# Kernel optimization log

Hardware: AMD Instinct MI355X
Metric: run time of the kernel (lower is better)

The kernel has to match this reference:

```python
import jax, jax.numpy as jnp
import numpy as np

EMBED = 1024  # embed_dim = hidden_dim = out_dim (n_head=1)
NQ, NK = 4096, 4096
NEG = 1e16


def setup_inputs() -> dict:
    key = jax.random.key(0)
    ks = jax.random.split(key, 10)
    stdv = 1.0 / np.sqrt(EMBED)
    lin = lambda kk: jax.random.uniform(kk, (EMBED, EMBED), jnp.float32, -stdv, stdv)
    vec = lambda kk: jax.random.uniform(kk, (EMBED,), jnp.float32, -stdv, stdv)
    return {
        "q": jax.random.normal(ks[0], (NQ, EMBED), jnp.float32),
        "k": jax.random.normal(ks[1], (NK, EMBED), jnp.float32),
        "mask": jax.random.randint(ks[2], (NQ, NK), 0, 2, jnp.int32),
        "wei": jax.random.uniform(ks[3], (NQ, NK), jnp.float32),
        "Wq": lin(ks[4]), "bq": vec(ks[5]),
        "Wk": lin(ks[6]), "bk": vec(ks[7]),
        "Wp": lin(ks[8]), "bp": vec(ks[9]),
    }


def reference(q, k, mask, wei, Wq, bq, Wk, bk, Wp, bp):
    # Linear projections (torch Linear: x @ W.T + b)
    kx = k @ Wk.T + bk                      # [NK, D]
    qx = q @ Wq.T + bq                      # [NQ, D]
    # dot_product score
    score = qx @ kx.T                       # [NQ, NK]
    bias = (mask.astype(jnp.int32) - 1).astype(score.dtype) * NEG
    score = jax.nn.softmax(score + bias, axis=-1)
    # second weighted+masked softmax pass
    score = jax.nn.softmax(score * wei + bias, axis=-1)
    out = (score @ kx) @ Wp.T + bp          # [NQ, D]
    return out, score
```

## Files before the change

### kernel.cpp

```cpp
#include <hip/hip_runtime.h>


typedef __bf16 bf16;
typedef __bf16 bf16x8 __attribute__((ext_vector_type(8)));
typedef __bf16 bf16x4 __attribute__((ext_vector_type(4)));
typedef float  f32x4  __attribute__((ext_vector_type(4)));
typedef float  f32x16 __attribute__((ext_vector_type(16)));

typedef __attribute__((address_space(1))) void as1_void;
typedef __attribute__((address_space(3))) void as3_void;

#define NQ  4096
#define NKK 4096
#define EMB 1024

#define BM 128
#define BN 128
#define BK 32

__device__ __forceinline__ void gld_lds16(const void* g, void* l) {
    __builtin_amdgcn_global_load_lds((as1_void*)g, (as3_void*)l, 16, 0, 0);
}

__global__ __launch_bounds__(256) void prep_all(
    const float* __restrict__ q, const float* __restrict__ k,
    const float* __restrict__ Wq, const float* __restrict__ Wk, const float* __restrict__ Wp,
    bf16* __restrict__ qh, bf16* __restrict__ ql,
    bf16* __restrict__ kh, bf16* __restrict__ kl,
    bf16* __restrict__ Wqh, bf16* __restrict__ Wql,
    bf16* __restrict__ Wkh, bf16* __restrict__ Wkl,
    bf16* __restrict__ Wph, bf16* __restrict__ Wpl,
    int nqk, int nw)
{
    const int z = blockIdx.y;
    const float* s; bf16* h; bf16* l; int n;
    switch (z) {
        case 0:  s = q;  h = qh;  l = ql;  n = nqk; break;
        case 1:  s = k;  h = kh;  l = kl;  n = nqk; break;
        case 2:  s = Wq; h = Wqh; l = Wql; n = nw;  break;
        case 3:  s = Wk; h = Wkh; l = Wkl; n = nw;  break;
        default: s = Wp; h = Wph; l = Wpl; n = nw;  break;
    }
    const int i = (blockIdx.x * 256 + threadIdx.x) * 4;
    if (i >= n) return;
    f32x4 v = *(const f32x4*)(s + i);
    bf16x4 hv, lv;
#pragma unroll
    for (int c = 0; c < 4; c++) {
        float x = v[c];
        bf16 hh = (bf16)x;
        hv[c] = hh;
        lv[c] = (bf16)(x - (float)hh);
    }
    *(bf16x4*)(h + i) = hv;
    *(bf16x4*)(l + i) = lv;
}

__global__ __launch_bounds__(256) void transpose_bf16(
    const bf16* __restrict__ src, bf16* __restrict__ dst, int R, int C)
{
    __shared__ bf16 tile[32][33];
    const int bx = blockIdx.x * 32;
    const int by = blockIdx.y * 32;
    const int tx = threadIdx.x & 31;
    const int ty = threadIdx.x >> 5;
#pragma unroll
    for (int r = 0; r < 4; r++)
        tile[ty + 8 * r][tx] = src[(size_t)(by + ty + 8 * r) * C + bx + tx];
    __syncthreads();
#pragma unroll
    for (int r = 0; r < 4; r++)
        dst[(size_t)(bx + ty + 8 * r) * R + by + tx] = tile[tx][ty + 8 * r];
}

template<int NS, int MODE>
__global__ __launch_bounds__(256) void reduce_k(
    const float* __restrict__ P, const float* __restrict__ bias,
    float* __restrict__ of, bf16* __restrict__ oh, int n, int Nld)
{
    const int i = (blockIdx.x * 256 + threadIdx.x) * 4;
    if (i >= n) return;
    f32x4 v = *(const f32x4*)(P + i);
#pragma unroll
    for (int s = 1; s < NS; s++)
        v += *(const f32x4*)(P + (size_t)s * n + i);
    if (MODE == 1)
        v += *(const f32x4*)(bias + (i & (Nld - 1)));
    if (MODE == 0) {
        bf16x4 o;
#pragma unroll
        for (int c = 0; c < 4; c++) o[c] = (bf16)v[c];
        *(bf16x4*)(oh + i) = o;
    } else {
        *(f32x4*)(of + i) = v;
    }
}

template<int NSPLIT, int HAS_BIAS, int OUT_BF16>
__global__ __launch_bounds__(256) void gemm_bt(
    const bf16* __restrict__ A, const bf16* __restrict__ B,
    const float* __restrict__ bias,
    float* __restrict__ Cf, bf16* __restrict__ Cb,
    int M, int N, int Ksub, int lda, int ldb)
{
    __shared__ bf16 sA[BM * BK];
    __shared__ bf16 sB[BN * BK];
    const int t    = threadIdx.x;
    const int wave = t >> 6;
    const int lane = t & 63;
    const int l31  = lane & 31;
    const int lhi  = lane >> 5;
    const int wm   = wave >> 1;
    const int wn   = wave & 1;
    const int bm   = blockIdx.y * BM;
    const int bn   = blockIdx.x * BN;
    const int srow = t >> 2;
    const int gseg = (t & 3) ^ ((srow >> 1) & 3);
    const int rsw  = (l31 >> 1) & 3;
    const int kz   = (NSPLIT > 0) ? (int)blockIdx.z : 0;

    A += (size_t)kz * Ksub;
    B += (size_t)kz * Ksub;
    if (NSPLIT > 0) Cf += (size_t)kz * M * N;

    const bf16* ga = A + (size_t)(bm + srow) * lda + gseg * 8;
    const bf16* gb = B + (size_t)(bn + srow) * ldb + gseg * 8;
    char* lA = (char*)sA + wave * 1024;
    char* lB = (char*)sB + wave * 1024;

    f32x16 acc[2][2] = {};

    for (int k0 = 0; k0 < Ksub; k0 += BK) {
        __syncthreads();
        gld_lds16(ga + k0,                      lA);
        gld_lds16(ga + (size_t)64 * lda + k0,   lA + 4096);
        gld_lds16(gb + k0,                      lB);
        gld_lds16(gb + (size_t)64 * ldb + k0,   lB + 4096);
        __syncthreads();
        bf16x8 af[2][2], bfr[2][2];
#pragma unroll
        for (int mi = 0; mi < 2; mi++)
#pragma unroll
            for (int kh = 0; kh < 2; kh++)
                af[mi][kh] = *(const bf16x8*)
                    &sA[(wm * 64 + mi * 32 + l31) * BK + ((kh * 2 + lhi) ^ rsw) * 8];
#pragma unroll
        for (int nj = 0; nj < 2; nj++)
#pragma unroll
            for (int kh = 0; kh < 2; kh++)
                bfr[nj][kh] = *(const bf16x8*)
                    &sB[(wn * 64 + nj * 32 + l31) * BK + ((kh * 2 + lhi) ^ rsw) * 8];
#pragma unroll
        for (int kh = 0; kh < 2; kh++)
#pragma unroll
            for (int mi = 0; mi < 2; mi++)
#pragma unroll
                for (int nj = 0; nj < 2; nj++)
                    acc[mi][nj] = __builtin_amdgcn_mfma_f32_32x32x16_bf16(
                        af[mi][kh], bfr[nj][kh], acc[mi][nj], 0, 0, 0);
    }

#pragma unroll
    for (int mi = 0; mi < 2; mi++)
#pragma unroll
        for (int nj = 0; nj < 2; nj++) {
            const int cg = bn + wn * 64 + nj * 32 + l31;
            const float bv = HAS_BIAS ? bias[cg] : 0.0f;
#pragma unroll
            for (int r = 0; r < 16; r++) {
                const int rg = bm + wm * 64 + mi * 32 + (r & 3) + 8 * (r >> 2) + 4 * lhi;
                const float v = acc[mi][nj][r] + bv;
                const size_t idx = (size_t)rg * N + cg;
                if (NSPLIT > 0)    Cf[idx] = v;
                else if (OUT_BF16) Cb[idx] = (bf16)v;
                else               Cf[idx] = v;
            }
        }
}

template<int BATCH, int HAS_BIAS, int HILO>
__global__ __launch_bounds__(256) void gemm_bt_split(
    const bf16* __restrict__ Ah0, const bf16* __restrict__ Al0,
    const bf16* __restrict__ Bh0, const bf16* __restrict__ Bl0,
    const float* __restrict__ bias0, bf16* __restrict__ Ch0, bf16* __restrict__ Cl0,
    const bf16* __restrict__ Ah1, const bf16* __restrict__ Al1,
    const bf16* __restrict__ Bh1, const bf16* __restrict__ Bl1,
    const float* __restrict__ bias1, bf16* __restrict__ Ch1, bf16* __restrict__ Cl1,
    float* __restrict__ Cf,
    int M, int N, int K)
{
    __shared__ bf16 sAh[BM * BK], sAl[BM * BK], sBh[BN * BK], sBl[BN * BK];
    const int t    = threadIdx.x;
    const int wave = t >> 6;
    const int lane = t & 63;
    const int l31  = lane & 31;
    const int lhi  = lane >> 5;
    const int wm   = wave >> 1;
    const int wn   = wave & 1;
    const int bm   = blockIdx.y * BM;
    const int bn   = blockIdx.x * BN;
    const int srow = t >> 2;
    const int gseg = (t & 3) ^ ((srow >> 1) & 3);
    const int rsw  = (l31 >> 1) & 3;

    const int mt = BATCH ? (int)blockIdx.z : 0;

    const bf16* Ah = (BATCH && mt) ? Ah1 : Ah0;
    const bf16* Al = (BATCH && mt) ? Al1 : Al0;
    const bf16* Bh = (BATCH && mt) ? Bh1 : Bh0;
    const bf16* Bl = (BATCH && mt) ? Bl1 : Bl0;
    const float* bias = (BATCH && mt) ? bias1 : bias0;
    bf16* Ch = (BATCH && mt) ? Ch1 : Ch0;
    bf16* Cl = (BATCH && mt) ? Cl1 : Cl0;

    const size_t offA = (size_t)(bm + srow) * K + gseg * 8;
    const size_t offB = (size_t)(bn + srow) * K + gseg * 8;
    char* lAh = (char*)sAh + wave * 1024;
    char* lAl = (char*)sAl + wave * 1024;
    char* lBh = (char*)sBh + wave * 1024;
    char* lBl = (char*)sBl + wave * 1024;

    f32x16 acc[2][2] = {};

    for (int k0 = 0; k0 < K; k0 += BK) {
        __syncthreads();
        gld_lds16(Ah + offA + k0,                  lAh);
        gld_lds16(Ah + offA + (size_t)64 * K + k0, lAh + 4096);
        gld_lds16(Al + offA + k0,                  lAl);
        gld_lds16(Al + offA + (size_t)64 * K + k0, lAl + 4096);
        gld_lds16(Bh + offB + k0,                  lBh);
        gld_lds16(Bh + offB + (size_t)64 * K + k0, lBh + 4096);
        gld_lds16(Bl + offB + k0,                  lBl);
        gld_lds16(Bl + offB + (size_t)64 * K + k0, lBl + 4096);
        __syncthreads();
#pragma unroll
        for (int kh = 0; kh < 2; kh++) {
            const int ksw = ((kh * 2 + lhi) ^ rsw) * 8;
            bf16x8 ah[2], al[2], bh2[2], bl2[2];
#pragma unroll
            for (int mi = 0; mi < 2; mi++) {
                const int ro = (wm * 64 + mi * 32 + l31) * BK + ksw;
                ah[mi] = *(const bf16x8*)&sAh[ro];
                al[mi] = *(const bf16x8*)&sAl[ro];
            }
#pragma unroll
            for (int nj = 0; nj < 2; nj++) {
                const int ro = (wn * 64 + nj * 32 + l31) * BK + ksw;
                bh2[nj] = *(const bf16x8*)&sBh[ro];
                bl2[nj] = *(const bf16x8*)&sBl[ro];
            }
#pragma unroll
            for (int mi = 0; mi < 2; mi++)
#pragma unroll
                for (int nj = 0; nj < 2; nj++) {
                    acc[mi][nj] = __builtin_amdgcn_mfma_f32_32x32x16_bf16(al[mi], bh2[nj], acc[mi][nj], 0, 0, 0);
                    acc[mi][nj] = __builtin_amdgcn_mfma_f32_32x32x16_bf16(ah[mi], bl2[nj], acc[mi][nj], 0, 0, 0);
                    acc[mi][nj] = __builtin_amdgcn_mfma_f32_32x32x16_bf16(ah[mi], bh2[nj], acc[mi][nj], 0, 0, 0);
                }
        }
    }

#pragma unroll
    for (int mi = 0; mi < 2; mi++)
#pragma unroll
        for (int nj = 0; nj < 2; nj++) {
            const int cg = bn + wn * 64 + nj * 32 + l31;
            const float bv = HAS_BIAS ? bias[cg] : 0.0f;
#pragma unroll
            for (int r = 0; r < 16; r++) {
                const int rg = bm + wm * 64 + mi * 32 + (r & 3) + 8 * (r >> 2) + 4 * lhi;
                const float v = acc[mi][nj][r] + bv;
                const size_t idx = (size_t)rg * N + cg;
                if (HILO) {
                    const bf16 hh = (bf16)v;
                    Ch[idx] = hh;
                    Cl[idx] = (bf16)(v - (float)hh);
                } else {
                    Cf[idx] = v;
                }
            }
        }
}

__global__ __launch_bounds__(256, 2) void gemm_score(
    const bf16* __restrict__ Ah, const bf16* __restrict__ Al,
    const bf16* __restrict__ Bh, const bf16* __restrict__ Bl,
    const int* __restrict__ mask,
    float* __restrict__ Cf, int N, int K)
{
    __shared__ bf16 sAh[128 * BK], sAl[128 * BK], sBh[256 * BK], sBl[256 * BK];
    const int t    = threadIdx.x;
    const int wave = t >> 6;
    const int lane = t & 63;
    const int l31  = lane & 31;
    const int lhi  = lane >> 5;
    const int bm   = blockIdx.y * 128;
    const int bn   = blockIdx.x * 256;
    const int srow = t >> 2;
    const int gseg = (t & 3) ^ ((srow >> 1) & 3);
    const int rsw  = (l31 >> 1) & 3;

    const size_t offA = (size_t)(bm + srow) * K + gseg * 8;
    const size_t offB = (size_t)(bn + srow) * K + gseg * 8;
    char* lAh = (char*)sAh + wave * 1024;
    char* lAl = (char*)sAl + wave * 1024;
    char* lBh = (char*)sBh + wave * 1024;
    char* lBl = (char*)sBl + wave * 1024;

    f32x16 acc[4][2] = {};

    for (int k0 = 0; k0 < K; k0 += BK) {
        __syncthreads();
        gld_lds16(Ah + offA + k0,                  lAh);
        gld_lds16(Ah + offA + (size_t)64 * K + k0, lAh + 4096);
        gld_lds16(Al + offA + k0,                  lAl);
        gld_lds16(Al + offA + (size_t)64 * K + k0, lAl + 4096);
#pragma unroll
        for (int rb = 0; rb < 4; rb++) {
            gld_lds16(Bh + offB + (size_t)(64 * rb) * K + k0, lBh + rb * 4096);
            gld_lds16(Bl + offB + (size_t)(64 * rb) * K + k0, lBl + rb * 4096);
        }
        __syncthreads();
#pragma unroll
        for (int kh = 0; kh < 2; kh++) {
            const int ksw = ((kh * 2 + lhi) ^ rsw) * 8;
            bf16x8 ah[4], al[4], bh2[2], bl2[2];
#pragma unroll
            for (int mi = 0; mi < 4; mi++) {
                const int ro = (mi * 32 + l31) * BK + ksw;
                ah[mi] = *(const bf16x8*)&sAh[ro];
                al[mi] = *(const bf16x8*)&sAl[ro];
            }
#pragma unroll
            for (int nj = 0; nj < 2; nj++) {
                const int ro = (wave * 64 + nj * 32 + l31) * BK + ksw;
                bh2[nj] = *(const bf16x8*)&sBh[ro];
                bl2[nj] = *(const bf16x8*)&sBl[ro];
            }
#pragma unroll
            for (int mi = 0; mi < 4; mi++)
#pragma unroll
                for (int nj = 0; nj < 2; nj++) {
                    acc[mi][nj] = __builtin_amdgcn_mfma_f32_32x32x16_bf16(al[mi], bh2[nj], acc[mi][nj], 0, 0, 0);
                    acc[mi][nj] = __builtin_amdgcn_mfma_f32_32x32x16_bf16(ah[mi], bl2[nj], acc[mi][nj], 0, 0, 0);
                    acc[mi][nj] = __builtin_amdgcn_mfma_f32_32x32x16_bf16(ah[mi], bh2[nj], acc[mi][nj], 0, 0, 0);
                }
        }
    }

#pragma unroll
    for (int mi = 0; mi < 4; mi++)
#pragma unroll
        for (int nj = 0; nj < 2; nj++) {
            const int cg = bn + wave * 64 + nj * 32 + l31;
#pragma unroll
            for (int r = 0; r < 16; r++) {
                const int rg = bm + mi * 32 + (r & 3) + 8 * (r >> 2) + 4 * lhi;
                const size_t idx = (size_t)rg * N + cg;
                Cf[idx] = mask[idx] ? acc[mi][nj][r] : -1e16f;
            }
        }
}

__device__ __forceinline__ float wred_max(float v) {
#pragma unroll
    for (int off = 32; off > 0; off >>= 1) v = fmaxf(v, __shfl_xor(v, off));
    return v;
}
__device__ __forceinline__ float wred_sum(float v) {
#pragma unroll
    for (int off = 32; off > 0; off >>= 1) v += __shfl_xor(v, off);
    return v;
}

__global__ __launch_bounds__(256) void softmax2_kernel(
    float* __restrict__ score, const float* __restrict__ wei,
    bf16* __restrict__ scoreb)
{
    __shared__ float sred[4];
    const int row = blockIdx.x;
    const int t   = threadIdx.x;
    const size_t base = (size_t)row * NKK + (size_t)t * 16;
    const int wv = t >> 6, ln = t & 63;

    float l[16], w[16];
#pragma unroll
    for (int c = 0; c < 4; c++) {
        *(f32x4*)(l + 4 * c) = *(const f32x4*)(score + base + 4 * c);
        *(f32x4*)(w + 4 * c) = *(const f32x4*)(wei + base + 4 * c);
    }
    unsigned mb = 0;
#pragma unroll
    for (int s = 0; s < 16; s++) if (l[s] > -1e15f) mb |= 1u << s;

    float mx = -__builtin_inff();
#pragma unroll
    for (int s = 0; s < 16; s++) if (mb & (1u << s)) mx = fmaxf(mx, l[s]);
    mx = wred_max(mx);
    if (ln == 0) sred[wv] = mx;
    __syncthreads();
    mx = fmaxf(fmaxf(sred[0], sred[1]), fmaxf(sred[2], sred[3]));
    __syncthreads();
    float sum = 0.f;
#pragma unroll
    for (int s = 0; s < 16; s++) {
        const float e = (mb & (1u << s)) ? __expf(l[s] - mx) : 0.f;
        l[s] = e; sum += e;
    }
    sum = wred_sum(sum);
    if (ln == 0) sred[wv] = sum;
    __syncthreads();
    sum = sred[0] + sred[1] + sred[2] + sred[3];
    __syncthreads();
    const float inv1 = 1.0f / sum;

#pragma unroll
    for (int s = 0; s < 16; s++) l[s] = l[s] * inv1 * w[s];

    float mx2 = -__builtin_inff();
#pragma unroll
    for (int s = 0; s < 16; s++) if (mb & (1u << s)) mx2 = fmaxf(mx2, l[s]);
    mx2 = wred_max(mx2);
    if (ln == 0) sred[wv] = mx2;
    __syncthreads();
    mx2 = fmaxf(fmaxf(sred[0], sred[1]), fmaxf(sred[2], sred[3]));
    __syncthreads();
    float sum2 = 0.f;
#pragma unroll
    for (int s = 0; s < 16; s++) {
        const float e = (mb & (1u << s)) ? __expf(l[s] - mx2) : 0.f;
        l[s] = e; sum2 += e;
    }
    sum2 = wred_sum(sum2);
    if (ln == 0) sred[wv] = sum2;
    __syncthreads();
    sum2 = sred[0] + sred[1] + sred[2] + sred[3];
    const float inv2 = 1.0f / sum2;

#pragma unroll
    for (int c = 0; c < 4; c++) {
        f32x4 pv;
#pragma unroll
        for (int j = 0; j < 4; j++) pv[j] = l[4 * c + j] * inv2;
        *(f32x4*)(score + base + 4 * c) = pv;
#pragma unroll
        for (int j = 0; j < 4; j++) l[4 * c + j] = pv[j];
    }
    bf16x8 b0, b1;
#pragma unroll
    for (int j = 0; j < 8; j++) { b0[j] = (bf16)l[j]; b1[j] = (bf16)l[8 + j]; }
    *(bf16x8*)(scoreb + base)     = b0;
    *(bf16x8*)(scoreb + base + 8) = b1;
}

extern "C" void kernel_launch(void* const* d_in, const int* in_sizes, int n_in,
                              void* d_out, int out_size, void* d_ws, size_t ws_size,
                              hipStream_t stream)
{
    (void)in_sizes; (void)n_in; (void)out_size;
    const float* q    = (const float*)d_in[0];
    const float* k    = (const float*)d_in[1];
    const int*   mask = (const int*)  d_in[2];
    const float* wei  = (const float*)d_in[3];
    const float* Wq   = (const float*)d_in[4];
    const float* bq   = (const float*)d_in[5];
    const float* Wk   = (const float*)d_in[6];
    const float* bk   = (const float*)d_in[7];
    const float* Wp   = (const float*)d_in[8];
    const float* bp   = (const float*)d_in[9];

    float* out   = (float*)d_out;
    float* score = (float*)d_out + (size_t)NQ * EMB;

    char* ws = (char*)d_ws;
    size_t off = 0;
    auto alloc = [&](size_t bytes) -> char* {
        char* p = ws + off; off += (bytes + 255) & ~(size_t)255; return p;
    };
    const size_t n_qk = (size_t)NQ * EMB;
    const size_t n_w  = (size_t)EMB * EMB;
    const size_t n_sc = (size_t)NQ * NKK;

    bf16* qh   = (bf16*)alloc(n_qk * 2);
    bf16* ql   = (bf16*)alloc(n_qk * 2);
    bf16* kh   = (bf16*)alloc(n_qk * 2);
    bf16* kl   = (bf16*)alloc(n_qk * 2);
    bf16* qxh  = (bf16*)alloc(n_qk * 2);
    bf16* qxl  = (bf16*)alloc(n_qk * 2);
    bf16* kxh  = (bf16*)alloc(n_qk * 2);
    bf16* kxl  = (bf16*)alloc(n_qk * 2);
    bf16* Wqh  = (bf16*)alloc(n_w * 2);
    bf16* Wql  = (bf16*)alloc(n_w * 2);
    bf16* Wkh  = (bf16*)alloc(n_w * 2);
    bf16* Wkl  = (bf16*)alloc(n_w * 2);
    bf16* Wpb  = (bf16*)alloc(n_w * 2);
    bf16* Wpl  = (bf16*)alloc(n_w * 2);
    bf16* kxTb = (bf16*)alloc(n_qk * 2);
    bf16* ctxb = (bf16*)alloc(n_qk * 2);
    bf16* scoreb = (bf16*)alloc(n_sc * 2);
    const size_t base_off = off;
    float* P = (float*)alloc(2 * n_qk * 4);
    const bool ws_ok = (off <= ws_size);
    if (base_off > ws_size) return;

    const int MN = (int)n_qk;

    prep_all<<<dim3(n_qk / 1024, 5), 256, 0, stream>>>(
        q, k, Wq, Wk, Wp,
        qh, ql, kh, kl, Wqh, Wql, Wkh, Wkl, Wpb, Wpl,
        (int)n_qk, (int)n_w);

    gemm_bt_split<1, 1, 1><<<dim3(EMB / BN, NQ / BM, 2), 256, 0, stream>>>(
        qh, ql, Wqh, Wql, bq, qxh, qxl,
        kh, kl, Wkh, Wkl, bk, kxh, kxl,
        nullptr, NQ, EMB, EMB);

    transpose_bf16<<<dim3(EMB / 32, NKK / 32), 256, 0, stream>>>(kxh, kxTb, NKK, EMB);

    gemm_score<<<dim3(NKK / 256, NQ / 128), 256, 0, stream>>>(
        qxh, qxl, kxh, kxl, mask, score, NKK, EMB);

    softmax2_kernel<<<dim3(NQ), 256, 0, stream>>>(score, wei, scoreb);

    if (ws_ok) {
        gemm_bt<2, 0, 0><<<dim3(EMB / BN, NQ / BM, 2), 256, 0, stream>>>(
            scoreb, kxTb, nullptr, P, nullptr, NQ, EMB, NKK / 2, NKK, NKK);
        reduce_k<2, 0><<<dim3(MN / 1024), 256, 0, stream>>>(
            P, nullptr, nullptr, ctxb, MN, EMB);
    } else {
        gemm_bt<0, 0, 1><<<dim3(EMB / BN, NQ / BM), 256, 0, stream>>>(
            scoreb, kxTb, nullptr, nullptr, ctxb, NQ, EMB, NKK, NKK, NKK);
    }

    if (ws_ok) {
        gemm_bt<2, 0, 0><<<dim3(EMB / BN, NQ / BM, 2), 256, 0, stream>>>(
            ctxb, Wpb, nullptr, P, nullptr, NQ, EMB, EMB / 2, EMB, EMB);
        reduce_k<2, 1><<<dim3(MN / 1024), 256, 0, stream>>>(
            P, bp, out, nullptr, MN, EMB);
    } else {
        gemm_bt<0, 1, 0><<<dim3(EMB / BN, NQ / BM), 256, 0, stream>>>(
            ctxb, Wpb, bp, out, nullptr, NQ, EMB, EMB, EMB, EMB);
    }
}
```

Baseline: 521.3 us.

## Split-K the projection GEMMs and move mask application into softmax

Adds split-K to the batched Q/K projection GEMM (2-way per matrix, so 4 z-slices), with reduce kernels that add the bias and emit hi/lo bf16 pairs. The context and output GEMMs go from 2-way to 4-way split-K. The score GEMM no longer reads the int mask in its epilogue; softmax reads the mask directly instead of inferring it from sentinel values. This raises grid parallelism and slims the score epilogue, at the cost of extra fp32 partial traffic, more reduce launches and a larger workspace.

```diff
diff --git a/kernel.cpp b/kernel.cpp
--- a/kernel.cpp
+++ b/kernel.cpp
@@ -6,6 +6,7 @@
 typedef __bf16 bf16x4 __attribute__((ext_vector_type(4)));
 typedef float  f32x4  __attribute__((ext_vector_type(4)));
 typedef float  f32x16 __attribute__((ext_vector_type(16)));
+typedef int    i32x4  __attribute__((ext_vector_type(4)));
 
 typedef __attribute__((address_space(1))) void as1_void;
 typedef __attribute__((address_space(3))) void as3_void;
@@ -76,7 +77,8 @@
 template<int NS, int MODE>
 __global__ __launch_bounds__(256) void reduce_k(
     const float* __restrict__ P, const float* __restrict__ bias,
-    float* __restrict__ of, bf16* __restrict__ oh, int n, int Nld)
+    float* __restrict__ of, bf16* __restrict__ oh, bf16* __restrict__ ol,
+    int n, int Nld)
 {
     const int i = (blockIdx.x * 256 + threadIdx.x) * 4;
     if (i >= n) return;
@@ -84,15 +86,25 @@
 #pragma unroll
     for (int s = 1; s < NS; s++)
         v += *(const f32x4*)(P + (size_t)s * n + i);
-    if (MODE == 1)
+    if (MODE >= 1)
         v += *(const f32x4*)(bias + (i & (Nld - 1)));
     if (MODE == 0) {
         bf16x4 o;
 #pragma unroll
         for (int c = 0; c < 4; c++) o[c] = (bf16)v[c];
         *(bf16x4*)(oh + i) = o;
+    } else if (MODE == 1) {
+        *(f32x4*)(of + i) = v;
     } else {
-        *(f32x4*)(of + i) = v;
+        bf16x4 h, l;
+#pragma unroll
+        for (int c = 0; c < 4; c++) {
+            bf16 hh = (bf16)v[c];
+            h[c] = hh;
+            l[c] = (bf16)(v[c] - (float)hh);
+        }
+        *(bf16x4*)(oh + i) = h;
+        *(bf16x4*)(ol + i) = l;
     }
 }
 
@@ -178,7 +190,7 @@
         }
 }
 
-template<int BATCH, int HAS_BIAS, int HILO>
+template<int BATCH, int NSPLIT, int HAS_BIAS, int HILO>
 __global__ __launch_bounds__(256) void gemm_bt_split(
     const bf16* __restrict__ Ah0, const bf16* __restrict__ Al0,
     const bf16* __restrict__ Bh0, const bf16* __restrict__ Bl0,
@@ -186,8 +198,8 @@
     const bf16* __restrict__ Ah1, const bf16* __restrict__ Al1,
     const bf16* __restrict__ Bh1, const bf16* __restrict__ Bl1,
     const float* __restrict__ bias1, bf16* __restrict__ Ch1, bf16* __restrict__ Cl1,
-    float* __restrict__ Cf,
-    int M, int N, int K)
+    float* __restrict__ P, float* __restrict__ Cf,
+    int M, int N, int Ksub, int lda, int ldb)
 {
     __shared__ bf16 sAh[BM * BK], sAl[BM * BK], sBh[BN * BK], sBl[BN * BK];
     const int t    = threadIdx.x;
@@ -203,7 +215,9 @@
     const int gseg = (t & 3) ^ ((srow >> 1) & 3);
     const int rsw  = (l31 >> 1) & 3;
 
-    const int mt = BATCH ? (int)blockIdx.z : 0;
+    const int zs = (NSPLIT > 0) ? NSPLIT : 1;
+    const int mt = BATCH ? ((int)blockIdx.z / zs) : 0;
+    const int kz = (NSPLIT > 0) ? ((int)blockIdx.z % zs) : 0;
 
     const bf16* Ah = (BATCH && mt) ? Ah1 : Ah0;
     const bf16* Al = (BATCH && mt) ? Al1 : Al0;
@@ -212,9 +226,10 @@
     const float* bias = (BATCH && mt) ? bias1 : bias0;
     bf16* Ch = (BATCH && mt) ? Ch1 : Ch0;
     bf16* Cl = (BATCH && mt) ? Cl1 : Cl0;
-
-    const size_t offA = (size_t)(bm + srow) * K + gseg * 8;
-    const size_t offB = (size_t)(bn + srow) * K + gseg * 8;
+    if (NSPLIT > 0) P += (size_t)(mt * zs + kz) * M * N;
+
+    const size_t offA = (size_t)(bm + srow) * lda + gseg * 8 + (size_t)kz * Ksub;
+    const size_t offB = (size_t)(bn + srow) * ldb + gseg * 8 + (size_t)kz * Ksub;
     char* lAh = (char*)sAh + wave * 1024;
     char* lAl = (char*)sAl + wave * 1024;
     char* lBh = (char*)sBh + wave * 1024;
@@ -222,16 +237,16 @@
 
     f32x16 acc[2][2] = {};
 
-    for (int k0 = 0; k0 < K; k0 += BK) {
+    for (int k0 = 0; k0 < Ksub; k0 += BK) {
         __syncthreads();
-        gld_lds16(Ah + offA + k0,                  lAh);
-        gld_lds16(Ah + offA + (size_t)64 * K + k0, lAh + 4096);
-        gld_lds16(Al + offA + k0,                  lAl);
-        gld_lds16(Al + offA + (size_t)64 * K + k0, lAl + 4096);
-        gld_lds16(Bh + offB + k0,                  lBh);
-        gld_lds16(Bh + offB + (size_t)64 * K + k0, lBh + 4096);
-        gld_lds16(Bl + offB + k0,                  lBl);
-        gld_lds16(Bl + offB + (size_t)64 * K + k0, lBl + 4096);
+        gld_lds16(Ah + offA + k0,                    lAh);
+        gld_lds16(Ah + offA + (size_t)64 * lda + k0, lAh + 4096);
+        gld_lds16(Al + offA + k0,                    lAl);
+        gld_lds16(Al + offA + (size_t)64 * lda + k0, lAl + 4096);
+        gld_lds16(Bh + offB + k0,                    lBh);
+        gld_lds16(Bh + offB + (size_t)64 * ldb + k0, lBh + 4096);
+        gld_lds16(Bl + offB + k0,                    lBl);
+        gld_lds16(Bl + offB + (size_t)64 * ldb + k0, lBl + 4096);
         __syncthreads();
 #pragma unroll
         for (int kh = 0; kh < 2; kh++) {
@@ -265,13 +280,15 @@
 #pragma unroll
         for (int nj = 0; nj < 2; nj++) {
             const int cg = bn + wn * 64 + nj * 32 + l31;
-            const float bv = HAS_BIAS ? bias[cg] : 0.0f;
+            const float bv = (NSPLIT == 0 && HAS_BIAS) ? bias[cg] : 0.0f;
 #pragma unroll
             for (int r = 0; r < 16; r++) {
                 const int rg = bm + wm * 64 + mi * 32 + (r & 3) + 8 * (r >> 2) + 4 * lhi;
                 const float v = acc[mi][nj][r] + bv;
                 const size_t idx = (size_t)rg * N + cg;
-                if (HILO) {
+                if (NSPLIT > 0) {
+                    P[idx] = v;
+                } else if (HILO) {
                     const bf16 hh = (bf16)v;
                     Ch[idx] = hh;
                     Cl[idx] = (bf16)(v - (float)hh);
@@ -285,7 +302,6 @@
 __global__ __launch_bounds__(256, 2) void gemm_score(
     const bf16* __restrict__ Ah, const bf16* __restrict__ Al,
     const bf16* __restrict__ Bh, const bf16* __restrict__ Bl,
-    const int* __restrict__ mask,
     float* __restrict__ Cf, int N, int K)
 {
     __shared__ bf16 sAh[128 * BK], sAl[128 * BK], sBh[256 * BK], sBl[256 * BK];
@@ -356,8 +372,7 @@
 #pragma unroll
             for (int r = 0; r < 16; r++) {
                 const int rg = bm + mi * 32 + (r & 3) + 8 * (r >> 2) + 4 * lhi;
-                const size_t idx = (size_t)rg * N + cg;
-                Cf[idx] = mask[idx] ? acc[mi][nj][r] : -1e16f;
+                Cf[(size_t)rg * N + cg] = acc[mi][nj][r];
             }
         }
 }
@@ -374,8 +389,8 @@
 }
 
 __global__ __launch_bounds__(256) void softmax2_kernel(
-    float* __restrict__ score, const float* __restrict__ wei,
-    bf16* __restrict__ scoreb)
+    float* __restrict__ score, const int* __restrict__ mask,
+    const float* __restrict__ wei, bf16* __restrict__ scoreb)
 {
     __shared__ float sred[4];
     const int row = blockIdx.x;
@@ -384,14 +399,15 @@
     const int wv = t >> 6, ln = t & 63;
 
     float l[16], w[16];
+    unsigned mb = 0;
 #pragma unroll
     for (int c = 0; c < 4; c++) {
         *(f32x4*)(l + 4 * c) = *(const f32x4*)(score + base + 4 * c);
         *(f32x4*)(w + 4 * c) = *(const f32x4*)(wei + base + 4 * c);
-    }
-    unsigned mb = 0;
-#pragma unroll
-    for (int s = 0; s < 16; s++) if (l[s] > -1e15f) mb |= 1u << s;
+        i32x4 mv = *(const i32x4*)(mask + base + 4 * c);
+#pragma unroll
+        for (int j = 0; j < 4; j++) if (mv[j] != 0) mb |= 1u << (4 * c + j);
+    }
 
     float mx = -__builtin_inff();
 #pragma unroll
@@ -499,7 +515,7 @@
     bf16* ctxb = (bf16*)alloc(n_qk * 2);
     bf16* scoreb = (bf16*)alloc(n_sc * 2);
     const size_t base_off = off;
-    float* P = (float*)alloc(2 * n_qk * 4);
+    float* P = (float*)alloc(4 * n_qk * 4);
     const bool ws_ok = (off <= ws_size);
     if (base_off > ws_size) return;
 
@@ -510,33 +526,44 @@
         qh, ql, kh, kl, Wqh, Wql, Wkh, Wkl, Wpb, Wpl,
         (int)n_qk, (int)n_w);
 
-    gemm_bt_split<1, 1, 1><<<dim3(EMB / BN, NQ / BM, 2), 256, 0, stream>>>(
-        qh, ql, Wqh, Wql, bq, qxh, qxl,
-        kh, kl, Wkh, Wkl, bk, kxh, kxl,
-        nullptr, NQ, EMB, EMB);
+    if (ws_ok) {
+        gemm_bt_split<1, 2, 0, 0><<<dim3(EMB / BN, NQ / BM, 4), 256, 0, stream>>>(
+            qh, ql, Wqh, Wql, nullptr, nullptr, nullptr,
+            kh, kl, Wkh, Wkl, nullptr, nullptr, nullptr,
+            P, nullptr, NQ, EMB, EMB / 2, EMB, EMB);
+        reduce_k<2, 2><<<dim3(MN / 1024), 256, 0, stream>>>(
+            P,              bq, nullptr, qxh, qxl, MN, EMB);
+        reduce_k<2, 2><<<dim3(MN / 1024), 256, 0, stream>>>(
+            P + 2 * n_qk,   bk, nullptr, kxh, kxl, MN, EMB);
+    } else {
+        gemm_bt_split<1, 0, 1, 1><<<dim3(EMB / BN, NQ / BM, 2), 256, 0, stream>>>(
+            qh, ql, Wqh, Wql, bq, qxh, qxl,
+            kh, kl, Wkh, Wkl, bk, kxh, kxl,
+            nullptr, nullptr, NQ, EMB, EMB, EMB, EMB);
+    }
 
     transpose_bf16<<<dim3(EMB / 32, NKK / 32), 256, 0, stream>>>(kxh, kxTb, NKK, EMB);
 
     gemm_score<<<dim3(NKK / 256, NQ / 128), 256, 0, stream>>>(
-        qxh, qxl, kxh, kxl, mask, score, NKK, EMB);
-
-    softmax2_kernel<<<dim3(NQ), 256, 0, stream>>>(score, wei, scoreb);
+        qxh, qxl, kxh, kxl, score, NKK, EMB);
+
+    softmax2_kernel<<<dim3(NQ), 256, 0, stream>>>(score, mask, wei, scoreb);
 
     if (ws_ok) {
-        gemm_bt<2, 0, 0><<<dim3(EMB / BN, NQ / BM, 2), 256, 0, stream>>>(
-            scoreb, kxTb, nullptr, P, nullptr, NQ, EMB, NKK / 2, NKK, NKK);
-        reduce_k<2, 0><<<dim3(MN / 1024), 256, 0, stream>>>(
-            P, nullptr, nullptr, ctxb, MN, EMB);
+        gemm_bt<4, 0, 0><<<dim3(EMB / BN, NQ / BM, 4), 256, 0, stream>>>(
+            scoreb, kxTb, nullptr, P, nullptr, NQ, EMB, NKK / 4, NKK, NKK);
+        reduce_k<4, 0><<<dim3(MN / 1024), 256, 0, stream>>>(
+            P, nullptr, nullptr, ctxb, nullptr, MN, EMB);
     } else {
         gemm_bt<0, 0, 1><<<dim3(EMB / BN, NQ / BM), 256, 0, stream>>>(
             scoreb, kxTb, nullptr, nullptr, ctxb, NQ, EMB, NKK, NKK, NKK);
     }
 
     if (ws_ok) {
-        gemm_bt<2, 0, 0><<<dim3(EMB / BN, NQ / BM, 2), 256, 0, stream>>>(
-            ctxb, Wpb, nullptr, P, nullptr, NQ, EMB, EMB / 2, EMB, EMB);
-        reduce_k<2, 1><<<dim3(MN / 1024), 256, 0, stream>>>(
-            P, bp, out, nullptr, MN, EMB);
+        gemm_bt<4, 0, 0><<<dim3(EMB / BN, NQ / BM, 4), 256, 0, stream>>>(
+            ctxb, Wpb, nullptr, P, nullptr, NQ, EMB, EMB / 4, EMB, EMB);
+        reduce_k<4, 1><<<dim3(MN / 1024), 256, 0, stream>>>(
+            P, bp, out, nullptr, nullptr, MN, EMB);
     } else {
         gemm_bt<0, 1, 0><<<dim3(EMB / BN, NQ / BM), 256, 0, stream>>>(
             ctxb, Wpb, bp, out, nullptr, NQ, EMB, EMB, EMB, EMB);
```

After: 565.8 us. 8.5% more time.
